# Kernel optimization log

Hardware: AMD Instinct MI355X
Metric: run time of the kernel (lower is better)

The kernel has to match this reference:

```python
import jax, jax.numpy as jnp
import numpy as np

C = 256
WT_LEVELS = 3
SQ = 0.7071067811865476  # 1/sqrt(2), Haar/db1 coefficient
# Filters exactly as stored in the torch module (pywt db1, dec filters reversed):
DEC_LO = jnp.array([SQ, SQ], dtype=jnp.float32)
DEC_HI = jnp.array([SQ, -SQ], dtype=jnp.float32)
REC_LO = jnp.array([SQ, SQ], dtype=jnp.float32)
REC_HI = jnp.array([SQ, -SQ], dtype=jnp.float32)


def _conv_same(x, w, groups):
    # torch F.conv1d(padding='same'): total pad = k-1, left = total//2, rest right
    k = w.shape[-1]
    total = k - 1
    pad = (total // 2, total - total // 2)
    return jax.lax.conv_general_dilated(
        x, w, window_strides=(1,), padding=[pad],
        dimension_numbers=('NCH', 'OIH', 'NCH'),
        feature_group_count=groups)


def _dw_filter(filt, c):
    # depthwise weight [C, 1, k] from a 1D filter, matching .expand(C, -1, -1)
    return jnp.broadcast_to(filt.reshape(1, 1, -1), (c, 1, filt.shape[0]))


def _dwt(x):
    c = x.shape[1]
    lo = _conv_same(x, _dw_filter(DEC_LO, c), c)[:, :, ::2]
    hi = _conv_same(x, _dw_filter(DEC_HI, c), c)[:, :, ::2]
    return lo, hi


def _idwt(lo, hi):
    c = lo.shape[1]
    lo = jnp.repeat(lo, 2, axis=2)  # F.interpolate nearest, scale_factor=2
    hi = jnp.repeat(hi, 2, axis=2)
    lo = _conv_same(lo, _dw_filter(REC_LO, c), c)
    hi = _conv_same(hi, _dw_filter(REC_HI, c), c)
    m = min(lo.shape[2], hi.shape[2])
    return lo[:, :, :m] + hi[:, :, :m]


def setup_inputs() -> dict:
    key = jax.random.key(0)
    ks = jax.random.split(key, 7)
    B, L, K = 8, 16384, 5
    x = jax.random.normal(ks[0], (B, C, L), dtype=jnp.float32)
    conv_w = jax.random.normal(ks[1], (C, C, K), dtype=jnp.float32) * 0.05
    conv_b = jax.random.normal(ks[2], (C,), dtype=jnp.float32) * 0.05
    wconv0 = jax.random.normal(ks[3], (C, 1, K), dtype=jnp.float32) * 0.2
    wconv1 = jax.random.normal(ks[4], (C, 1, K), dtype=jnp.float32) * 0.2
    wconv2 = jax.random.normal(ks[5], (C, 1, K), dtype=jnp.float32) * 0.2
    scale = jnp.ones((1, C, 1), dtype=jnp.float32)
    return {"x": x, "conv_w": conv_w, "conv_b": conv_b,
            "wconv0": wconv0, "wconv1": wconv1, "wconv2": wconv2,
            "scale": scale}


def reference(x, conv_w, conv_b, wconv0, wconv1, wconv2, scale):
    # main full conv (groups=1, bias)
    out = _conv_same(x, conv_w, 1) + conv_b[None, :, None]

    # wavelet decomposition: dets collected finest->coarsest
    a = x
    dets = []
    for _ in range(WT_LEVELS):
        a, d = _dwt(a)
        dets.append(d)
    # coeffs[::-1] = [approx, d_coarsest, ..., d_finest];
    # wavelet_convs[i] applied in that order
    d_coarse = _conv_same(dets[2], wconv0, C)
    d_mid = _conv_same(dets[1], wconv1, C)
    d_fine = _conv_same(dets[0], wconv2, C)

    rec = _idwt(a, d_coarse)
    rec = _idwt(rec, d_mid)
    rec = _idwt(rec, d_fine)
    # L divisible by 2**WT_LEVELS -> rec length == orig length (no interpolate)

    return out + scale * rec
```

## Files before the change

kernel.cpp:

```cpp
#include <hip/hip_runtime.h>
#include <hip/hip_bf16.h>
#include <stdint.h>

#define SQF 0.70710678118654752f
#define SQ2 1.41421356237309505f

typedef __bf16 bf16x8 __attribute__((ext_vector_type(8)));
typedef float f32x4 __attribute__((ext_vector_type(4)));

using GLp = const __attribute__((address_space(1))) void*;
using LDp = __attribute__((address_space(3))) void*;

__device__ __forceinline__ unsigned short f2bf(float f) {
  union { float f; uint32_t u; } v; v.f = f;
  uint32_t r = v.u + 0x7fffu + ((v.u >> 16) & 1u);
  return (unsigned short)(r >> 16);
}
__device__ __forceinline__ float bf2f(unsigned short h) {
  union { uint32_t u; float f; } v; v.u = (uint32_t)h << 16; return v.f;
}

__global__ void prepack_w(const float* __restrict__ w, unsigned short* __restrict__ Wp) {
  int f = blockIdx.x * 256 + threadIdx.x;
  if (f >= 40 * 8192) return;
  int e = f & 7;
  int lane = (f >> 3) & 63;
  int cog = (f >> 9) & 15;
  int ks = f >> 13;
  int co = cog * 16 + (lane & 15);
  int ci = (ks & 7) * 32 + (lane >> 4) * 8 + e;
  int k = ks >> 3;
  Wp[f] = f2bf(w[(co * 256 + ci) * 5 + k]);
}

__global__ void transpose_x(const float* __restrict__ x, unsigned short* __restrict__ xT) {
  __shared__ __attribute__((aligned(16))) unsigned short Ts[64 * 72];
  const int lt = blockIdx.x, ct = blockIdx.y, b = blockIdx.z;
  const int t = threadIdx.x;
  const int l0 = lt * 64, ci0 = ct * 64;
#pragma unroll
  for (int p = 0; p < 4; ++p) {
    int cil = p * 16 + (t >> 4);
    int ll = (t & 15) * 4;
    const float4 v = *(const float4*)(x + (((size_t)b * 256 + ci0 + cil) * 16384 + l0 + ll));
    Ts[(ll + 0) * 72 + cil] = f2bf(v.x);
    Ts[(ll + 1) * 72 + cil] = f2bf(v.y);
    Ts[(ll + 2) * 72 + cil] = f2bf(v.z);
    Ts[(ll + 3) * 72 + cil] = f2bf(v.w);
  }
  __syncthreads();
#pragma unroll
  for (int p = 0; p < 4; ++p) {
    int ll = p * 16 + (t >> 4);
    int cq = (t & 15) * 4;
    ushort4 v = *(const ushort4*)(&Ts[ll * 72 + cq]);
    *(ushort4*)(xT + (((size_t)b * 16384 + l0 + ll) * 256 + ci0 + cq)) = v;
  }
}

__global__ __launch_bounds__(512, 4)
void conv_mfma(const unsigned short* __restrict__ xT, const unsigned short* __restrict__ Wp,
               const float* __restrict__ bias, float* __restrict__ out) {
  __shared__ __attribute__((aligned(16))) unsigned short Xs[132 * 256];
  const int tid = threadIdx.x;
  const int lane = tid & 63;
  const int wv = tid >> 6;
  const int wm = wv & 3;
  const int wn = wv >> 2;
  const int lt = blockIdx.x;
  const int b = blockIdx.y;
  const int l0 = lt << 7;
  const int r15 = lane & 15, g = lane >> 4;

  if (lt == 0 && tid < 64) *(float4*)(&Xs[tid * 8]) = float4{0.f, 0.f, 0.f, 0.f};
  if (lt == 127 && tid < 64) *(float4*)(&Xs[130 * 256 + tid * 8]) = float4{0.f, 0.f, 0.f, 0.f};

  {
    const size_t xbase = (size_t)b * 16384 * 256;
#pragma unroll
    for (int it = 0; it < 9; ++it) {
      int idx = it * 512 + tid;
      if (idx >= 132 * 32) break;
      int row = idx >> 5, cl = idx & 31;
      int l = l0 - 2 + row;
      void* ldst = (void*)(Xs + ((idx & ~63) << 3));
      if (l >= 0 && l < 16384) {
        const unsigned short* src = xT + xbase + (size_t)l * 256 + ((cl ^ (row & 7)) << 3);
        __builtin_amdgcn_global_load_lds((GLp)src, (LDp)ldst, 16, 0, 0);
      }
    }
  }

  auto loadA = [&](bf16x8* a, int ks) {
#pragma unroll
    for (int mf = 0; mf < 4; ++mf)
      a[mf] = *reinterpret_cast<const bf16x8*>(
          Wp + (size_t)ks * 8192 + ((wm * 4 + mf) << 9) + (lane << 3));
  };
  auto loadB = [&](bf16x8* bv, int ks) {
    const int k = ks >> 3, cb = ks & 7;
    const int c = cb * 4 + g;
    const int jb = wn * 64 + r15 + k;
#pragma unroll
    for (int nf = 0; nf < 4; ++nf) {
      int j = jb + nf * 16;
      bv[nf] = *reinterpret_cast<const bf16x8*>(&Xs[j * 256 + ((c ^ (j & 7)) << 3)]);
    }
  };

  f32x4 acc[4][4];
#pragma unroll
  for (int mf = 0; mf < 4; ++mf)
#pragma unroll
    for (int nf = 0; nf < 4; ++nf) acc[mf][nf] = f32x4{0.f, 0.f, 0.f, 0.f};

  bf16x8 aA[4], aB[4], bfr[4];
  loadA(aA, 0);
  __syncthreads();

  for (int ks = 0; ks < 40; ks += 2) {
    loadA(aB, ks + 1);
    loadB(bfr, ks);
#pragma unroll
    for (int mf = 0; mf < 4; ++mf)
#pragma unroll
      for (int nf = 0; nf < 4; ++nf)
        acc[mf][nf] = __builtin_amdgcn_mfma_f32_16x16x32_bf16(aA[mf], bfr[nf], acc[mf][nf], 0, 0, 0);
    if (ks < 38) loadA(aA, ks + 2);
    loadB(bfr, ks + 1);
#pragma unroll
    for (int mf = 0; mf < 4; ++mf)
#pragma unroll
      for (int nf = 0; nf < 4; ++nf)
        acc[mf][nf] = __builtin_amdgcn_mfma_f32_16x16x32_bf16(aB[mf], bfr[nf], acc[mf][nf], 0, 0, 0);
  }

  const size_t ob = (size_t)b * 256 * 16384;
  const int lglob = l0 + wn * 64 + r15;
#pragma unroll
  for (int mf = 0; mf < 4; ++mf) {
    int co0 = wm * 64 + mf * 16 + g * 4;
#pragma unroll
    for (int r = 0; r < 4; ++r) {
      float bv = bias[co0 + r];
#pragma unroll
      for (int nf = 0; nf < 4; ++nf)
        out[ob + (size_t)(co0 + r) * 16384 + lglob + nf * 16] = acc[mf][nf][r] + bv;
    }
  }
}

__global__ void conv_naive(const float* __restrict__ x, const float* __restrict__ w,
                           const float* __restrict__ bias, float* __restrict__ out) {
  int l = blockIdx.x * 256 + threadIdx.x;
  int co = blockIdx.y, b = blockIdx.z;
  float acc = bias[co];
  const float* xb = x + (size_t)b * 256 * 16384;
  const float* wr = w + (size_t)co * 256 * 5;
  for (int ci = 0; ci < 256; ++ci) {
    const float* xc = xb + (size_t)ci * 16384;
    const float* wc = wr + ci * 5;
#pragma unroll
    for (int k = 0; k < 5; ++k) {
      int j = l + k - 2;
      float v = (j >= 0 && j < 16384) ? xc[j] : 0.f;
      acc += wc[k] * v;
    }
  }
  out[((size_t)b * 256 + co) * 16384 + l] = acc;
}

#define OFF_D2  0
#define OFF_R1  4096
#define OFF_A3  8192
#define OFF_D3  10240
#define OFF_R2O 8192

__device__ __forceinline__ float conv5(const float* a, const float* w, int idx, int len) {
  if (idx >= len) return 0.f;
  float s = 0.f;
#pragma unroll
  for (int t = 0; t < 5; ++t) {
    int j = idx + t - 2;
    float v = (j >= 0 && j < len) ? a[j] : 0.f;
    s += w[t] * v;
  }
  return s;
}
__device__ __forceinline__ float conv5h(const unsigned short* a, const float* w, int idx, int len) {
  if (idx >= len) return 0.f;
  float s = 0.f;
#pragma unroll
  for (int t = 0; t < 5; ++t) {
    int j = idx + t - 2;
    float v = (j >= 0 && j < len) ? bf2f(a[j]) : 0.f;
    s += w[t] * v;
  }
  return s;
}

__global__ __launch_bounds__(1024, 2)
void wavelet_add(const float* __restrict__ x, const float* __restrict__ w0g,
                 const float* __restrict__ w1g, const float* __restrict__ w2g,
                 const float* __restrict__ scale, float* __restrict__ out) {
  __shared__ __attribute__((aligned(16))) unsigned short D1h[8192];
  __shared__ __attribute__((aligned(16))) float S[12288];
  const int t = threadIdx.x;
  const int bc = blockIdx.x;
  const int c = bc & 255;
  const size_t rowbase = (size_t)bc * 16384;
  float w0[5], w1[5], w2[5];
#pragma unroll
  for (int i = 0; i < 5; ++i) { w0[i] = w0g[c * 5 + i]; w1[i] = w1g[c * 5 + i]; w2[i] = w2g[c * 5 + i]; }
  const float sc = scale[c];

  {
    const float4* x4 = (const float4*)(x + rowbase);
    const int i0 = t, i1 = t + 1024;
    float4 u0 = x4[2 * i0];
    float4 v0 = x4[2 * i0 + 1];
    float4 u1 = x4[2 * i1];
    float4 v1 = x4[2 * i1 + 1];
#pragma unroll
    for (int s = 0; s < 2; ++s) {
      int i = s ? i1 : i0;
      float4 u = s ? u1 : u0;
      float4 v = s ? v1 : v0;
      float a10 = SQF * (u.x + u.y), d10 = SQF * (u.x - u.y);
      float a11 = SQF * (u.z + u.w), d11 = SQF * (u.z - u.w);
      float a12 = SQF * (v.x + v.y), d12 = SQF * (v.x - v.y);
      float a13 = SQF * (v.z + v.w), d13 = SQF * (v.z - v.w);
      uint32_t q0 = ((uint32_t)f2bf(d11) << 16) | f2bf(d10);
      uint32_t q1 = ((uint32_t)f2bf(d13) << 16) | f2bf(d12);
      *(uint2*)(&D1h[4 * i]) = uint2{q0, q1};
      float a20 = SQF * (a10 + a11), d20 = SQF * (a10 - a11);
      float a21 = SQF * (a12 + a13), d21 = SQF * (a12 - a13);
      *(float2*)(&S[OFF_D2 + 2 * i]) = float2{d20, d21};
      S[OFF_A3 + i] = SQF * (a20 + a21);
      S[OFF_D3 + i] = SQF * (a20 - a21);
    }
  }
  __syncthreads();
  {
    const float* A3 = &S[OFF_A3]; const float* D3 = &S[OFF_D3];
#pragma unroll
    for (int s = 0; s < 2; ++s) {
      int i = s * 1024 + t;
      float a3 = A3[i];
      float a3p = (i < 2047) ? A3[i + 1] : 0.f;
      float dc = conv5(D3, w0, i, 2048);
      float dcp = conv5(D3, w0, i + 1, 2048);
      *(float2*)(&S[OFF_R1 + 2 * i]) = float2{SQ2 * a3, SQF * (a3 + a3p + dc - dcp)};
    }
  }
  __syncthreads();
  {
    const float* R1 = &S[OFF_R1]; const float* D2 = &S[OFF_D2];
#pragma unroll
    for (int s = 0; s < 4; ++s) {
      int i = s * 1024 + t;
      float r1 = R1[i];
      float r1p = (i < 4095) ? R1[i + 1] : 0.f;
      float dm = conv5(D2, w1, i, 4096);
      float dmp = conv5(D2, w1, i + 1, 4096);
      S[OFF_R2O + i] = SQF * (r1 + r1p + dm - dmp);
    }
  }
  __syncthreads();
  {
    const float* R1 = &S[OFF_R1]; const float* R2O = &S[OFF_R2O];
    float4* op = (float4*)(out + rowbase);
#pragma unroll
    for (int s = 0; s < 4; ++s) {
      int m = s * 1024 + t;
      float r1 = R1[m];
      float r1p = (m < 4095) ? R1[m + 1] : 0.f;
      float ro = R2O[m];
      float e0 = SQ2 * r1;
      float e1 = SQ2 * r1p;
      float df0 = conv5h(D1h, w2, 2 * m, 8192);
      float df1 = conv5h(D1h, w2, 2 * m + 1, 8192);
      float df2 = conv5h(D1h, w2, 2 * m + 2, 8192);
      float4 cu = op[m];
      cu.x += sc * (SQ2 * e0);
      cu.y += sc * (SQF * (e0 + ro + df0 - df1));
      cu.z += sc * (SQ2 * ro);
      cu.w += sc * (SQF * (ro + e1 + df1 - df2));
      op[m] = cu;
    }
  }
}

extern "C" void kernel_launch(void* const* d_in, const int* in_sizes, int n_in,
                              void* d_out, int out_size, void* d_ws, size_t ws_size,
                              hipStream_t stream) {
  const float* x = (const float*)d_in[0];
  const float* conv_w = (const float*)d_in[1];
  const float* conv_b = (const float*)d_in[2];
  const float* w0 = (const float*)d_in[3];
  const float* w1 = (const float*)d_in[4];
  const float* w2 = (const float*)d_in[5];
  const float* scale = (const float*)d_in[6];
  float* out = (float*)d_out;

  const size_t XT_BYTES = 67108864ull;
  const size_t WP_BYTES = 655360ull;
  if (ws_size >= XT_BYTES + WP_BYTES) {
    unsigned short* xT = (unsigned short*)d_ws;
    unsigned short* Wp = (unsigned short*)((char*)d_ws + XT_BYTES);
    prepack_w<<<dim3(1280), dim3(256), 0, stream>>>(conv_w, Wp);
    transpose_x<<<dim3(256, 4, 8), dim3(256), 0, stream>>>(x, xT);
    conv_mfma<<<dim3(128, 8), dim3(512), 0, stream>>>(xT, Wp, conv_b, out);
  } else {
    conv_naive<<<dim3(64, 256, 8), dim3(256), 0, stream>>>(x, conv_w, conv_b, out);
  }
  wavelet_add<<<dim3(2048), dim3(1024), 0, stream>>>(x, w0, w1, w2, scale, out);
}
```

Before: 183.6 us.

## Double the sequence tile per block so each weight fragment feeds two tiles

Each conv block now covers 256 sequence positions instead of 128. It keeps two accumulator sets and reuses each loaded weight fragment for both halves, which halves global weight reads per output. The cost is double the LDS tile, twice the accumulator registers (launch bounds lowered to 2 blocks per CU), and half as many blocks (512), which cuts occupancy and leaves fewer blocks to spread across CUs.

```diff
diff --git a/kernel.cpp b/kernel.cpp
--- a/kernel.cpp
+++ b/kernel.cpp
@@ -58,29 +58,29 @@
   }
 }
 
-__global__ __launch_bounds__(512, 4)
+__global__ __launch_bounds__(512, 2)
 void conv_mfma(const unsigned short* __restrict__ xT, const unsigned short* __restrict__ Wp,
                const float* __restrict__ bias, float* __restrict__ out) {
-  __shared__ __attribute__((aligned(16))) unsigned short Xs[132 * 256];
+  __shared__ __attribute__((aligned(16))) unsigned short Xs[260 * 256];
   const int tid = threadIdx.x;
   const int lane = tid & 63;
   const int wv = tid >> 6;
   const int wm = wv & 3;
   const int wn = wv >> 2;
-  const int lt = blockIdx.x;
+  const int lt2 = blockIdx.x;
   const int b = blockIdx.y;
-  const int l0 = lt << 7;
+  const int l0 = lt2 << 8;
   const int r15 = lane & 15, g = lane >> 4;
 
-  if (lt == 0 && tid < 64) *(float4*)(&Xs[tid * 8]) = float4{0.f, 0.f, 0.f, 0.f};
-  if (lt == 127 && tid < 64) *(float4*)(&Xs[130 * 256 + tid * 8]) = float4{0.f, 0.f, 0.f, 0.f};
+  if (lt2 == 0 && tid < 64) *(float4*)(&Xs[tid * 8]) = float4{0.f, 0.f, 0.f, 0.f};
+  if (lt2 == 63 && tid < 64) *(float4*)(&Xs[258 * 256 + tid * 8]) = float4{0.f, 0.f, 0.f, 0.f};
 
   {
     const size_t xbase = (size_t)b * 16384 * 256;
 #pragma unroll
-    for (int it = 0; it < 9; ++it) {
+    for (int it = 0; it < 17; ++it) {
       int idx = it * 512 + tid;
-      if (idx >= 132 * 32) break;
+      if (idx >= 260 * 32) break;
       int row = idx >> 5, cl = idx & 31;
       int l = l0 - 2 + row;
       void* ldst = (void*)(Xs + ((idx & ~63) << 3));
@@ -97,10 +97,10 @@
       a[mf] = *reinterpret_cast<const bf16x8*>(
           Wp + (size_t)ks * 8192 + ((wm * 4 + mf) << 9) + (lane << 3));
   };
-  auto loadB = [&](bf16x8* bv, int ks) {
+  auto loadB = [&](bf16x8* bv, int tt, int ks) {
     const int k = ks >> 3, cb = ks & 7;
     const int c = cb * 4 + g;
-    const int jb = wn * 64 + r15 + k;
+    const int jb = tt * 128 + wn * 64 + r15 + k;
 #pragma unroll
     for (int nf = 0; nf < 4; ++nf) {
       int j = jb + nf * 16;
@@ -108,44 +108,64 @@
     }
   };
 
-  f32x4 acc[4][4];
+  f32x4 acc0[4][4], acc1[4][4];
 #pragma unroll
   for (int mf = 0; mf < 4; ++mf)
 #pragma unroll
-    for (int nf = 0; nf < 4; ++nf) acc[mf][nf] = f32x4{0.f, 0.f, 0.f, 0.f};
-
-  bf16x8 aA[4], aB[4], bfr[4];
+    for (int nf = 0; nf < 4; ++nf) {
+      acc0[mf][nf] = f32x4{0.f, 0.f, 0.f, 0.f};
+      acc1[mf][nf] = f32x4{0.f, 0.f, 0.f, 0.f};
+    }
+
+  bf16x8 aA[4], aB[4], b0[4], b1[4];
   loadA(aA, 0);
   __syncthreads();
 
   for (int ks = 0; ks < 40; ks += 2) {
     loadA(aB, ks + 1);
-    loadB(bfr, ks);
+    loadB(b0, 0, ks);
+    loadB(b1, 1, ks);
 #pragma unroll
     for (int mf = 0; mf < 4; ++mf)
 #pragma unroll
       for (int nf = 0; nf < 4; ++nf)
-        acc[mf][nf] = __builtin_amdgcn_mfma_f32_16x16x32_bf16(aA[mf], bfr[nf], acc[mf][nf], 0, 0, 0);
+        acc0[mf][nf] = __builtin_amdgcn_mfma_f32_16x16x32_bf16(aA[mf], b0[nf], acc0[mf][nf], 0, 0, 0);
+#pragma unroll
+    for (int mf = 0; mf < 4; ++mf)
+#pragma unroll
+      for (int nf = 0; nf < 4; ++nf)
+        acc1[mf][nf] = __builtin_amdgcn_mfma_f32_16x16x32_bf16(aA[mf], b1[nf], acc1[mf][nf], 0, 0, 0);
     if (ks < 38) loadA(aA, ks + 2);
-    loadB(bfr, ks + 1);
+    loadB(b0, 0, ks + 1);
+    loadB(b1, 1, ks + 1);
 #pragma unroll
     for (int mf = 0; mf < 4; ++mf)
 #pragma unroll
       for (int nf = 0; nf < 4; ++nf)
-        acc[mf][nf] = __builtin_amdgcn_mfma_f32_16x16x32_bf16(aB[mf], bfr[nf], acc[mf][nf], 0, 0, 0);
+        acc0[mf][nf] = __builtin_amdgcn_mfma_f32_16x16x32_bf16(aB[mf], b0[nf], acc0[mf][nf], 0, 0, 0);
+#pragma unroll
+    for (int mf = 0; mf < 4; ++mf)
+#pragma unroll
+      for (int nf = 0; nf < 4; ++nf)
+        acc1[mf][nf] = __builtin_amdgcn_mfma_f32_16x16x32_bf16(aB[mf], b1[nf], acc1[mf][nf], 0, 0, 0);
   }
 
   const size_t ob = (size_t)b * 256 * 16384;
-  const int lglob = l0 + wn * 64 + r15;
-#pragma unroll
-  for (int mf = 0; mf < 4; ++mf) {
-    int co0 = wm * 64 + mf * 16 + g * 4;
-#pragma unroll
-    for (int r = 0; r < 4; ++r) {
-      float bv = bias[co0 + r];
-#pragma unroll
-      for (int nf = 0; nf < 4; ++nf)
-        out[ob + (size_t)(co0 + r) * 16384 + lglob + nf * 16] = acc[mf][nf][r] + bv;
+#pragma unroll
+  for (int tt = 0; tt < 2; ++tt) {
+    const int lglob = l0 + tt * 128 + wn * 64 + r15;
+#pragma unroll
+    for (int mf = 0; mf < 4; ++mf) {
+      int co0 = wm * 64 + mf * 16 + g * 4;
+#pragma unroll
+      for (int r = 0; r < 4; ++r) {
+        float bv = bias[co0 + r];
+#pragma unroll
+        for (int nf = 0; nf < 4; ++nf) {
+          float v = (tt == 0 ? acc0[mf][nf][r] : acc1[mf][nf][r]) + bv;
+          out[ob + (size_t)(co0 + r) * 16384 + lglob + nf * 16] = v;
+        }
+      }
     }
   }
 }
@@ -310,7 +330,7 @@
     unsigned short* Wp = (unsigned short*)((char*)d_ws + XT_BYTES);
     prepack_w<<<dim3(1280), dim3(256), 0, stream>>>(conv_w, Wp);
     transpose_x<<<dim3(256, 4, 8), dim3(256), 0, stream>>>(x, xT);
-    conv_mfma<<<dim3(128, 8), dim3(512), 0, stream>>>(xT, Wp, conv_b, out);
+    conv_mfma<<<dim3(64, 8), dim3(512), 0, stream>>>(xT, Wp, conv_b, out);
   } else {
     conv_naive<<<dim3(64, 256, 8), dim3(256), 0, stream>>>(x, conv_w, conv_b, out);
   }
```

After: 186.4 us. Within noise of the previous version (+1.5%).
